# Kernel tuning notes

Measured on AMD Instinct MI355X. Metric: run time of the kernel, lower is better.

## Reference

```python
import jax, jax.numpy as jnp
import numpy as np

DIM = 128
NUM_HEADS = 2
WS = 8  # window_size


def setup_inputs() -> dict:
    key = jax.random.key(0)
    ks = jax.random.split(key, 8)
    B, C, H, W = 1, DIM, 64, 128  # W must equal DIM (proj acts on last spatial axis)
    w_scale = 1.0 / np.sqrt(DIM)
    return {
        "x": jax.random.normal(ks[0], (B, C, H, W), jnp.float32),
        "wavelet_features": jax.random.normal(ks[1], (B, C, H, W), jnp.float32),
        "Wq": jax.random.normal(ks[2], (DIM, DIM), jnp.float32) * w_scale,
        "bq": jnp.zeros((DIM,), jnp.float32),
        "Wk": jax.random.normal(ks[3], (DIM, DIM), jnp.float32) * w_scale,
        "bk": jnp.zeros((DIM,), jnp.float32),
        "Wv": jax.random.normal(ks[4], (DIM, DIM), jnp.float32) * w_scale,
        "bv": jnp.zeros((DIM,), jnp.float32),
        "Wp": jax.random.normal(ks[5], (DIM, DIM), jnp.float32) * w_scale,
        "bp": jnp.zeros((DIM,), jnp.float32),
    }


def _window_partition(t):
    # 'b c (h wh) (w ww) -> b (h w) (wh ww) c'
    B, C, H, W = t.shape
    h, w = H // WS, W // WS
    t = t.reshape(B, C, h, WS, w, WS)
    t = t.transpose(0, 2, 4, 3, 5, 1)  # B,h,w,wh,ww,C
    return t.reshape(B, h * w, WS * WS, C)


def reference(x, wavelet_features, Wq, bq, Wk, bk, Wv, bv, Wp, bp):
    B, C, H, W = x.shape
    hd = C // NUM_HEADS
    scale = hd ** (-0.5)

    xw = _window_partition(x)                   # [B, nW, ws*ws, C]
    ww = _window_partition(wavelet_features)    # [B, nW, ws*ws, C]

    q = xw @ Wq.T + bq
    k = ww @ Wk.T + bk
    v = ww @ Wv.T + bv

    # NOTE: original code flattens windows+tokens together, so attention is
    # GLOBAL over all N = H*W tokens (window partition is just a permutation).
    N = q.shape[1] * q.shape[2]
    q = q.reshape(B, N, NUM_HEADS, hd).transpose(0, 2, 1, 3)  # [B,h,N,d]
    k = k.reshape(B, N, NUM_HEADS, hd).transpose(0, 2, 1, 3)
    v = v.reshape(B, N, NUM_HEADS, hd).transpose(0, 2, 1, 3)

    attn = jax.nn.softmax(jnp.einsum('bhnd,bhmd->bhnm', q, k) * scale, axis=-1)
    out = jnp.einsum('bhnm,bhmd->bhnd', attn, v)  # [B,h,N,d]
    out = out.transpose(0, 2, 1, 3).reshape(B, N, C)

    # 'b (h w) (wh ww) c -> b c (h wh) (w ww)'
    h, w = H // WS, W // WS
    out = out.reshape(B, h, w, WS, WS, C).transpose(0, 5, 1, 3, 2, 4).reshape(B, C, H, W)

    # Faithful quirk: proj Linear acts on the LAST axis (spatial W == dim).
    out = out @ Wp.T + bp
    return out
```

## Files before the change

kernel.cpp:

```cpp
#include <hip/hip_runtime.h>
#include <stdint.h>

typedef float    f32x4  __attribute__((ext_vector_type(4)));
typedef __bf16   bf16x8 __attribute__((ext_vector_type(8)));
typedef short    s16x8  __attribute__((ext_vector_type(8)));
typedef int      i32x4  __attribute__((ext_vector_type(4)));
typedef unsigned short u16x4 __attribute__((ext_vector_type(4)));

#define DEVINL __device__ __forceinline__

DEVINL unsigned short f2bf(float f) {
  unsigned u = __builtin_bit_cast(unsigned, f);
  return (unsigned short)((u + 0x7fffu + ((u >> 16) & 1u)) >> 16);
}

DEVINL f32x4 mfma16(bf16x8 a, bf16x8 b, f32x4 c) {
  return __builtin_amdgcn_mfma_f32_16x16x32_bf16(a, b, c, 0, 0, 0);
}

DEVINL bf16x8 lds_frag(const unsigned char* p) {
  return __builtin_bit_cast(bf16x8, *(const s16x8*)p);
}

template <int CTRL>
DEVINL float dppf(float x) {
  int xi = __builtin_bit_cast(int, x);
  return __builtin_bit_cast(float, __builtin_amdgcn_update_dpp(xi, xi, CTRL, 0xF, 0xF, true));
}
DEVINL float redmax16(float v) {
  v = fmaxf(v, dppf<0xB1>(v));
  v = fmaxf(v, dppf<0x4E>(v));
  v = fmaxf(v, dppf<0x141>(v));
  v = fmaxf(v, dppf<0x140>(v));
  return v;
}
DEVINL float redsum16(float v) {
  v += dppf<0xB1>(v);
  v += dppf<0x4E>(v);
  v += dppf<0x141>(v);
  v += dppf<0x140>(v);
  return v;
}

__global__ __launch_bounds__(256) void prep_w_kernel(
    const float* __restrict__ wq, const float* __restrict__ wk,
    const float* __restrict__ wv, const float* __restrict__ wp,
    unsigned short* __restrict__ wbf) {
  int id = blockIdx.x * 256 + threadIdx.x;
  int m = id >> 12;
  const float* src = (m == 0) ? wq : (m == 1) ? wk : (m == 2) ? wv : wp;
  f32x4 v = ((const f32x4*)src)[id & 4095];
  u16x4 o;
  o[0] = f2bf(v[0]); o[1] = f2bf(v[1]); o[2] = f2bf(v[2]); o[3] = f2bf(v[3]);
  ((u16x4*)wbf)[id] = o;
}

__global__ __launch_bounds__(256) void qkv_kernel(
    const float* __restrict__ x, const float* __restrict__ wav,
    const unsigned short* __restrict__ wbf,
    const float* __restrict__ bq, const float* __restrict__ bk, const float* __restrict__ bv,
    unsigned short* __restrict__ Qb, unsigned short* __restrict__ Kb,
    unsigned short* __restrict__ Vt) {
  __shared__ __align__(16) unsigned char sm[32768];
  const int tid = threadIdx.x;
  const int g = blockIdx.x >> 7;
  const int s0 = (blockIdx.x & 127) * 64;
  const float* srcm = (g == 0) ? x : wav;

  {
    const int c = tid >> 1, half = tid & 1;
    const float* xs = srcm + c * 8192 + s0 + half * 32;
#pragma unroll
    for (int i = 0; i < 8; ++i) {
      f32x4 vx = *(const f32x4*)(xs + i * 4);
#pragma unroll
      for (int j = 0; j < 4; ++j) {
        int s = half * 32 + i * 4 + j;
        int off = (c * 2) ^ ((s & 7) << 4);
        *(unsigned short*)(sm + s * 256 + off) = f2bf(vx[j]);
      }
    }
  }
  __syncthreads();

  const int w = tid >> 6, l = tid & 63, lr = l & 15, lh = l >> 4;
  const int arow = w * 16 + lr;
  const int aswz = (lr & 7) << 4;

  const unsigned char* asrc = sm + arow * 256;
  const unsigned char* wsrc = (const unsigned char*)wbf + g * 32768;
  f32x4 acc[8];
#pragma unroll
  for (int jt = 0; jt < 8; ++jt) acc[jt] = (f32x4){0.f, 0.f, 0.f, 0.f};
#pragma unroll
  for (int ks = 0; ks < 4; ++ks) {
    bf16x8 a = lds_frag(asrc + ((ks * 64 + lh * 16) ^ aswz));
#pragma unroll
    for (int jt = 0; jt < 8; ++jt) {
      bf16x8 bb = __builtin_bit_cast(
          bf16x8, *(const s16x8*)(wsrc + (jt * 16 + lr) * 256 + ks * 64 + lh * 16));
      acc[jt] = mfma16(a, bb, acc[jt]);
    }
  }
  if (g < 2) {
    const float* bias = g ? bk : bq;
    unsigned short* outp = g ? Kb : Qb;
#pragma unroll
    for (int jt = 0; jt < 8; ++jt) {
      float bb = bias[jt * 16 + lr];
#pragma unroll
      for (int r = 0; r < 4; ++r) {
        int row = s0 + w * 16 + lh * 4 + r;
        outp[row * 128 + jt * 16 + lr] = f2bf(acc[jt][r] + bb);
      }
    }
  } else {
    unsigned char* sm2 = sm + 16384;
#pragma unroll
    for (int jt = 0; jt < 8; ++jt) {
      float bb = bv[jt * 16 + lr];
#pragma unroll
      for (int r = 0; r < 4; ++r) {
        int jj = jt * 16 + lr;
        int sl = w * 16 + lh * 4 + r;
        *(unsigned short*)(sm2 + jj * 128 + ((sl * 2) ^ ((jj & 7) << 4))) =
            f2bf(acc[jt][r] + bb);
      }
    }
    __syncthreads();
#pragma unroll
    for (int g2 = 0; g2 < 4; ++g2) {
      int jj = w * 32 + g2 * 8 + (l >> 3);
      s16x8 row = *(const s16x8*)(sm2 + jj * 128 + (((l & 7) * 16) ^ ((jj & 7) << 4)));
      *(s16x8*)(Vt + jj * 8192 + s0 + (l & 7) * 8) = row;
    }
  }
}

__global__ __launch_bounds__(256) void attn_kernel(
    const unsigned short* __restrict__ Qb, const unsigned short* __restrict__ Kb,
    const unsigned short* __restrict__ Vt, float* __restrict__ Opart,
    float* __restrict__ Ml, float* __restrict__ Ll, int TPS) {
  __shared__ __align__(16) unsigned char sm[24576];
  const int tid = threadIdx.x;
  const int bid = blockIdx.x;
  const int hq = bid & 255, sp = bid >> 8;
  const int h = hq & 1, q0 = (hq >> 1) * 64;
  const int t0 = sp * TPS;
  const int w = tid >> 6, l = tid & 63, lr = l & 15, lh = l >> 4;
  const int lswz = (lr & 7) << 4;

  bf16x8 qf[2];
#pragma unroll
  for (int ks = 0; ks < 2; ++ks)
    qf[ks] = __builtin_bit_cast(
        bf16x8, *(const s16x8*)(Qb + (q0 + w * 16 + lr) * 128 + h * 64 + ks * 32 + lh * 8));

  f32x4 acc[4];
  float m_[4], l_[4];
#pragma unroll
  for (int i = 0; i < 4; ++i) { acc[i] = (f32x4){0.f,0.f,0.f,0.f}; m_[i] = -1e30f; l_[i] = 0.f; }

  int srow[2], soff[2], sldsoff[2];
#pragma unroll
  for (int i = 0; i < 2; ++i) {
    int ch = tid + i * 256;
    srow[i] = ch >> 3;
    soff[i] = (ch & 7) * 8;
    sldsoff[i] = srow[i] * 128 + ((soff[i] * 2) ^ ((srow[i] & 7) << 4));
  }

  {
#pragma unroll
    for (int i = 0; i < 2; ++i) {
      i32x4 kv = *(const i32x4*)(Kb + (t0 * 64 + srow[i]) * 128 + h * 64 + soff[i]);
      i32x4 vv = *(const i32x4*)(Vt + (h * 64 + srow[i]) * 8192 + t0 * 64 + soff[i]);
      *(i32x4*)(sm + sldsoff[i]) = kv;
      *(i32x4*)(sm + 8192 + sldsoff[i]) = vv;
    }
  }
  __syncthreads();

  const float sc = 0.18033688011112042f;

  for (int tt = 0; tt < TPS; ++tt) {
    const int t = t0 + tt;
    i32x4 nk[2], nv[2];
    if (tt < TPS - 1) {
#pragma unroll
      for (int i = 0; i < 2; ++i) {
        nk[i] = *(const i32x4*)(Kb + ((t + 1) * 64 + srow[i]) * 128 + h * 64 + soff[i]);
        nv[i] = *(const i32x4*)(Vt + (h * 64 + srow[i]) * 8192 + (t + 1) * 64 + soff[i]);
      }
    }
    const unsigned char* kb = sm;
    const unsigned char* vb = sm + 8192;
    unsigned char* pb = sm + 16384;

    f32x4 s4[4];
#pragma unroll
    for (int nt = 0; nt < 4; ++nt) s4[nt] = (f32x4){0.f,0.f,0.f,0.f};
#pragma unroll
    for (int ks = 0; ks < 2; ++ks) {
#pragma unroll
      for (int nt = 0; nt < 4; ++nt) {
        bf16x8 kf = lds_frag(kb + (nt * 16 + lr) * 128 + ((ks * 64 + lh * 16) ^ lswz));
        s4[nt] = mfma16(qf[ks], kf, s4[nt]);
      }
    }

    float p[4][4];
#pragma unroll
    for (int r = 0; r < 4; ++r) {
      float mx = fmaxf(fmaxf(s4[0][r], s4[1][r]), fmaxf(s4[2][r], s4[3][r]));
      mx = redmax16(mx) * sc;
      float mn = fmaxf(m_[r], mx);
      float al = __builtin_amdgcn_exp2f(m_[r] - mn);
      m_[r] = mn;
      float rs = 0.f;
#pragma unroll
      for (int nt = 0; nt < 4; ++nt) {
        p[nt][r] = __builtin_amdgcn_exp2f(fmaf(s4[nt][r], sc, -mn));
        rs += p[nt][r];
      }
      rs = redsum16(rs);
      l_[r] = l_[r] * al + rs;
#pragma unroll
      for (int ct = 0; ct < 4; ++ct) acc[ct][r] *= al;
    }

    const int qrow = w * 16 + lh * 4;
#pragma unroll
    for (int r = 0; r < 4; r += 2) {
      int qa = qrow + r, qb2 = qrow + r + 1;
      unsigned char* rowa = pb + qa * 128;
      unsigned char* rowb = pb + qb2 * 128;
      int swza = (qa & 7) << 4, swzb = (qb2 & 7) << 4;
#pragma unroll
      for (int nt = 0; nt < 4; ++nt) {
        unsigned u;
        asm("v_cvt_pk_bf16_f32 %0, %1, %2" : "=v"(u) : "v"(p[nt][r]), "v"(p[nt][r + 1]));
        int koff = (nt * 16 + lr) * 2;
        *(unsigned short*)(rowa + (koff ^ swza)) = (unsigned short)u;
        *(unsigned short*)(rowb + (koff ^ swzb)) = (unsigned short)(u >> 16);
      }
    }
    asm volatile("s_waitcnt lgkmcnt(0)" ::: "memory");
    __builtin_amdgcn_sched_barrier(0);

    bf16x8 pa[2];
#pragma unroll
    for (int ks = 0; ks < 2; ++ks)
      pa[ks] = lds_frag(pb + (w * 16 + lr) * 128 + ((ks * 64 + lh * 16) ^ lswz));
#pragma unroll
    for (int ks = 0; ks < 2; ++ks) {
#pragma unroll
      for (int ct = 0; ct < 4; ++ct) {
        bf16x8 vf = lds_frag(vb + (ct * 16 + lr) * 128 + ((ks * 64 + lh * 16) ^ lswz));
        acc[ct] = mfma16(pa[ks], vf, acc[ct]);
      }
    }

    __syncthreads();
    if (tt < TPS - 1) {
#pragma unroll
      for (int i = 0; i < 2; ++i) {
        *(i32x4*)(sm + sldsoff[i]) = nk[i];
        *(i32x4*)(sm + 8192 + sldsoff[i]) = nv[i];
      }
    }
    __syncthreads();
  }

  float* op = Opart + (size_t)bid * 4096;
#pragma unroll
  for (int ct = 0; ct < 4; ++ct) {
#pragma unroll
    for (int r = 0; r < 4; ++r) {
      int q = w * 16 + lh * 4 + r;
      op[q * 64 + ct * 16 + lr] = acc[ct][r];
    }
  }
  if (lr == 0) {
#pragma unroll
    for (int r = 0; r < 4; ++r) {
      int q = w * 16 + lh * 4 + r;
      Ml[bid * 64 + q] = m_[r];
      Ll[bid * 64 + q] = l_[r];
    }
  }
}

__global__ __launch_bounds__(256) void combine_kernel(
    const float* __restrict__ Opart, const float* __restrict__ Ml,
    const float* __restrict__ Ll, unsigned short* __restrict__ Ot, int S) {
  __shared__ float wgt_s[8][32];
  __shared__ float rinv_s[32];
  __shared__ unsigned short lt[64][34];
  const int bid = blockIdx.x;
  const int hq = bid >> 1, half = bid & 1;
  const int h = hq & 1, q0 = (hq >> 1) * 64;
  const int t = threadIdx.x;

  if (t < 32) {
    int qg = half * 32 + t;
    float m8[8];
    float M = -1e30f;
    for (int sp = 0; sp < S; ++sp) {
      m8[sp] = Ml[(size_t)(sp * 256 + hq) * 64 + qg];
      M = fmaxf(M, m8[sp]);
    }
    float L = 0.f;
    for (int sp = 0; sp < S; ++sp) {
      float wv = __builtin_amdgcn_exp2f(m8[sp] - M);
      wgt_s[sp][t] = wv;
      L += Ll[(size_t)(sp * 256 + hq) * 64 + qg] * wv;
    }
    rinv_s[t] = 1.0f / L;
  }
  __syncthreads();

  const int q = t >> 3;
  const int dc = t & 7;
  const int qg = half * 32 + q;
  f32x4 o0 = (f32x4){0.f,0.f,0.f,0.f}, o1 = (f32x4){0.f,0.f,0.f,0.f};
  for (int sp = 0; sp < S; ++sp) {
    const f32x4* src =
        (const f32x4*)(Opart + (size_t)(sp * 256 + hq) * 4096 + qg * 64 + dc * 8);
    float wv = wgt_s[sp][q];
    o0 += src[0] * wv;
    o1 += src[1] * wv;
  }
  float rinv = rinv_s[q];
#pragma unroll
  for (int j = 0; j < 4; ++j) lt[dc * 8 + j][q] = f2bf(o0[j] * rinv);
#pragma unroll
  for (int j = 0; j < 4; ++j) lt[dc * 8 + 4 + j][q] = f2bf(o1[j] * rinv);
  __syncthreads();

  const int d = t >> 2, q8 = (t & 3) * 8;
  unsigned short tmp[8];
#pragma unroll
  for (int j = 0; j < 8; ++j) tmp[j] = lt[d][q8 + j];
  *(s16x8*)(Ot + (size_t)(h * 64 + d) * 8192 + q0 + half * 32 + q8) = *(s16x8*)tmp;
}

__global__ __launch_bounds__(256) void proj_kernel(
    const unsigned short* __restrict__ Ot, const unsigned short* __restrict__ wbf,
    const float* __restrict__ bp, float* __restrict__ out) {
  __shared__ __align__(16) unsigned char sm[16384];
  const int tid = threadIdx.x;
  const int r0 = blockIdx.x * 64;
#pragma unroll
  for (int i = 0; i < 4; ++i) {
    int chk = tid + 256 * i;
    i32x4 v = *(const i32x4*)(Ot + r0 * 128 + chk * 8);
    int row = chk >> 4, off = (chk & 15) * 16;
    *(i32x4*)(sm + row * 256 + (off ^ ((row & 7) << 4))) = v;
  }
  __syncthreads();
  const int w = tid >> 6, l = tid & 63, lr = l & 15, lh = l >> 4;
  f32x4 acc[8];
#pragma unroll
  for (int jt = 0; jt < 8; ++jt) acc[jt] = (f32x4){0.f, 0.f, 0.f, 0.f};
  const unsigned char* wsrc = (const unsigned char*)wbf + 3 * 32768;
#pragma unroll
  for (int ks = 0; ks < 4; ++ks) {
    bf16x8 a = lds_frag(sm + (w * 16 + lr) * 256 + ((ks * 64 + lh * 16) ^ ((lr & 7) << 4)));
#pragma unroll
    for (int jt = 0; jt < 8; ++jt) {
      bf16x8 bb = __builtin_bit_cast(
          bf16x8, *(const s16x8*)(wsrc + (jt * 16 + lr) * 256 + ks * 64 + lh * 16));
      acc[jt] = mfma16(a, bb, acc[jt]);
    }
  }
#pragma unroll
  for (int jt = 0; jt < 8; ++jt) {
    float bb = bp[jt * 16 + lr];
#pragma unroll
    for (int r = 0; r < 4; ++r)
      out[(r0 + w * 16 + lh * 4 + r) * 128 + jt * 16 + lr] = acc[jt][r] + bb;
  }
}

extern "C" void kernel_launch(void* const* d_in, const int* in_sizes, int n_in,
                              void* d_out, int out_size, void* d_ws, size_t ws_size,
                              hipStream_t stream) {
  const float* x   = (const float*)d_in[0];
  const float* wav = (const float*)d_in[1];
  const float* Wq  = (const float*)d_in[2];
  const float* bq  = (const float*)d_in[3];
  const float* Wk  = (const float*)d_in[4];
  const float* bk  = (const float*)d_in[5];
  const float* Wv  = (const float*)d_in[6];
  const float* bv  = (const float*)d_in[7];
  const float* Wp  = (const float*)d_in[8];
  const float* bp  = (const float*)d_in[9];
  (void)in_sizes; (void)n_in; (void)out_size;

  unsigned char* ws = (unsigned char*)d_ws;
  unsigned short* Qb  = (unsigned short*)(ws);
  unsigned short* Kb  = (unsigned short*)(ws + 2097152);
  unsigned short* Vt  = (unsigned short*)(ws + 4194304);
  unsigned short* Ot  = (unsigned short*)(ws + 6291456);
  unsigned short* Wbf = (unsigned short*)(ws + 8388608);

  const size_t pbase = 8519680;
  int S = 8;
  while (S > 1 && pbase + (size_t)S * 4325376 > ws_size) S >>= 1;
  float* Opart = (float*)(ws + pbase);
  float* Ml    = (float*)(ws + pbase + (size_t)S * 4194304);
  float* Ll    = (float*)(ws + pbase + (size_t)S * 4194304 + (size_t)S * 65536);
  const int TPS = 128 / S;

  prep_w_kernel<<<64, 256, 0, stream>>>(Wq, Wk, Wv, Wp, Wbf);
  qkv_kernel<<<384, 256, 0, stream>>>(x, wav, Wbf, bq, bk, bv, Qb, Kb, Vt);
  attn_kernel<<<256 * S, 256, 0, stream>>>(Qb, Kb, Vt, Opart, Ml, Ll, TPS);
  combine_kernel<<<512, 256, 0, stream>>>(Opart, Ml, Ll, Ot, S);
  proj_kernel<<<128, 256, 0, stream>>>(Ot, Wbf, bp, (float*)d_out);
}
```

Before: 122.9 us.

## Double attention KV tile to 128 keys and compute row sums via MFMA

The attention kernel now processes 128 keys per iteration instead of 64, halving loop iterations and the number of online-softmax rescale steps and barriers per block. The P tile overwrites the K region in LDS after an added barrier, so shared memory grows to 32 KB instead of 48 KB. The softmax row sum is no longer a DPP shuffle reduction; it is computed by an extra MFMA of P against a ones vector, using the bf16-rounded P values. This adds register pressure (8 score tiles) and an extra sync per iteration.

```diff
diff --git a/kernel.cpp b/kernel.cpp
--- a/kernel.cpp
+++ b/kernel.cpp
@@ -32,13 +32,6 @@
   v = fmaxf(v, dppf<0x4E>(v));
   v = fmaxf(v, dppf<0x141>(v));
   v = fmaxf(v, dppf<0x140>(v));
-  return v;
-}
-DEVINL float redsum16(float v) {
-  v += dppf<0xB1>(v);
-  v += dppf<0x4E>(v);
-  v += dppf<0x141>(v);
-  v += dppf<0x140>(v);
   return v;
 }
 
@@ -140,13 +133,13 @@
 __global__ __launch_bounds__(256) void attn_kernel(
     const unsigned short* __restrict__ Qb, const unsigned short* __restrict__ Kb,
     const unsigned short* __restrict__ Vt, float* __restrict__ Opart,
-    float* __restrict__ Ml, float* __restrict__ Ll, int TPS) {
-  __shared__ __align__(16) unsigned char sm[24576];
+    float* __restrict__ Ml, float* __restrict__ Ll, int NIT) {
+  __shared__ __align__(16) unsigned char sm[32768];
   const int tid = threadIdx.x;
   const int bid = blockIdx.x;
   const int hq = bid & 255, sp = bid >> 8;
   const int h = hq & 1, q0 = (hq >> 1) * 64;
-  const int t0 = sp * TPS;
+  const int t0 = sp * NIT;
   const int w = tid >> 6, l = tid & 63, lr = l & 15, lh = l >> 4;
   const int lswz = (lr & 7) << 4;
 
@@ -156,91 +149,94 @@
     qf[ks] = __builtin_bit_cast(
         bf16x8, *(const s16x8*)(Qb + (q0 + w * 16 + lr) * 128 + h * 64 + ks * 32 + lh * 8));
 
+  const s16x8 ones_i = {0x3F80, 0x3F80, 0x3F80, 0x3F80, 0x3F80, 0x3F80, 0x3F80, 0x3F80};
+  const bf16x8 onesf = __builtin_bit_cast(bf16x8, ones_i);
+
   f32x4 acc[4];
   float m_[4], l_[4];
 #pragma unroll
   for (int i = 0; i < 4; ++i) { acc[i] = (f32x4){0.f,0.f,0.f,0.f}; m_[i] = -1e30f; l_[i] = 0.f; }
 
-  int srow[2], soff[2], sldsoff[2];
-#pragma unroll
-  for (int i = 0; i < 2; ++i) {
+  int srow[4], soff[4], kldsoff[4], vrow[4], voff[4], vldsoff[4];
+#pragma unroll
+  for (int i = 0; i < 4; ++i) {
     int ch = tid + i * 256;
     srow[i] = ch >> 3;
     soff[i] = (ch & 7) * 8;
-    sldsoff[i] = srow[i] * 128 + ((soff[i] * 2) ^ ((srow[i] & 7) << 4));
+    kldsoff[i] = srow[i] * 128 + ((soff[i] * 2) ^ ((srow[i] & 7) << 4));
+    vrow[i] = ch >> 4;
+    voff[i] = (ch & 15) * 8;
+    vldsoff[i] = 16384 + vrow[i] * 256 + ((voff[i] * 2) ^ ((vrow[i] & 7) << 4));
   }
 
   {
 #pragma unroll
-    for (int i = 0; i < 2; ++i) {
-      i32x4 kv = *(const i32x4*)(Kb + (t0 * 64 + srow[i]) * 128 + h * 64 + soff[i]);
-      i32x4 vv = *(const i32x4*)(Vt + (h * 64 + srow[i]) * 8192 + t0 * 64 + soff[i]);
-      *(i32x4*)(sm + sldsoff[i]) = kv;
-      *(i32x4*)(sm + 8192 + sldsoff[i]) = vv;
+    for (int i = 0; i < 4; ++i) {
+      i32x4 kv = *(const i32x4*)(Kb + (size_t)(t0 * 128 + srow[i]) * 128 + h * 64 + soff[i]);
+      i32x4 vv = *(const i32x4*)(Vt + (size_t)(h * 64 + vrow[i]) * 8192 + t0 * 128 + voff[i]);
+      *(i32x4*)(sm + kldsoff[i]) = kv;
+      *(i32x4*)(sm + vldsoff[i]) = vv;
     }
   }
   __syncthreads();
 
   const float sc = 0.18033688011112042f;
 
-  for (int tt = 0; tt < TPS; ++tt) {
-    const int t = t0 + tt;
-    i32x4 nk[2], nv[2];
-    if (tt < TPS - 1) {
-#pragma unroll
-      for (int i = 0; i < 2; ++i) {
-        nk[i] = *(const i32x4*)(Kb + ((t + 1) * 64 + srow[i]) * 128 + h * 64 + soff[i]);
-        nv[i] = *(const i32x4*)(Vt + (h * 64 + srow[i]) * 8192 + (t + 1) * 64 + soff[i]);
-      }
-    }
-    const unsigned char* kb = sm;
-    const unsigned char* vb = sm + 8192;
-    unsigned char* pb = sm + 16384;
-
-    f32x4 s4[4];
-#pragma unroll
-    for (int nt = 0; nt < 4; ++nt) s4[nt] = (f32x4){0.f,0.f,0.f,0.f};
+  for (int tt = 0; tt < NIT; ++tt) {
+    i32x4 nk[4], nv[4];
+    if (tt < NIT - 1) {
+#pragma unroll
+      for (int i = 0; i < 4; ++i) {
+        nk[i] = *(const i32x4*)(Kb + (size_t)((t0 + tt + 1) * 128 + srow[i]) * 128 + h * 64 + soff[i]);
+        nv[i] = *(const i32x4*)(Vt + (size_t)(h * 64 + vrow[i]) * 8192 + (t0 + tt + 1) * 128 + voff[i]);
+      }
+    }
+    const unsigned char* kp = sm;
+    const unsigned char* vb = sm + 16384;
+
+    f32x4 s8[8];
+#pragma unroll
+    for (int nt = 0; nt < 8; ++nt) s8[nt] = (f32x4){0.f,0.f,0.f,0.f};
 #pragma unroll
     for (int ks = 0; ks < 2; ++ks) {
 #pragma unroll
-      for (int nt = 0; nt < 4; ++nt) {
-        bf16x8 kf = lds_frag(kb + (nt * 16 + lr) * 128 + ((ks * 64 + lh * 16) ^ lswz));
-        s4[nt] = mfma16(qf[ks], kf, s4[nt]);
-      }
-    }
-
-    float p[4][4];
+      for (int nt = 0; nt < 8; ++nt) {
+        bf16x8 kf = lds_frag(kp + (nt * 16 + lr) * 128 + ((ks * 64 + lh * 16) ^ lswz));
+        s8[nt] = mfma16(qf[ks], kf, s8[nt]);
+      }
+    }
+
 #pragma unroll
     for (int r = 0; r < 4; ++r) {
-      float mx = fmaxf(fmaxf(s4[0][r], s4[1][r]), fmaxf(s4[2][r], s4[3][r]));
+      float mx = s8[0][r];
+#pragma unroll
+      for (int nt = 1; nt < 8; ++nt) mx = fmaxf(mx, s8[nt][r]);
       mx = redmax16(mx) * sc;
       float mn = fmaxf(m_[r], mx);
       float al = __builtin_amdgcn_exp2f(m_[r] - mn);
       m_[r] = mn;
-      float rs = 0.f;
-#pragma unroll
-      for (int nt = 0; nt < 4; ++nt) {
-        p[nt][r] = __builtin_amdgcn_exp2f(fmaf(s4[nt][r], sc, -mn));
-        rs += p[nt][r];
-      }
-      rs = redsum16(rs);
-      l_[r] = l_[r] * al + rs;
+      l_[r] *= al;
+#pragma unroll
+      for (int nt = 0; nt < 8; ++nt)
+        s8[nt][r] = __builtin_amdgcn_exp2f(fmaf(s8[nt][r], sc, -mn));
 #pragma unroll
       for (int ct = 0; ct < 4; ++ct) acc[ct][r] *= al;
     }
+
+    __syncthreads();
 
     const int qrow = w * 16 + lh * 4;
 #pragma unroll
     for (int r = 0; r < 4; r += 2) {
       int qa = qrow + r, qb2 = qrow + r + 1;
-      unsigned char* rowa = pb + qa * 128;
-      unsigned char* rowb = pb + qb2 * 128;
+      unsigned char* rowa = sm + qa * 256;
+      unsigned char* rowb = sm + qb2 * 256;
       int swza = (qa & 7) << 4, swzb = (qb2 & 7) << 4;
 #pragma unroll
-      for (int nt = 0; nt < 4; ++nt) {
+      for (int nt = 0; nt < 8; ++nt) {
         unsigned u;
-        asm("v_cvt_pk_bf16_f32 %0, %1, %2" : "=v"(u) : "v"(p[nt][r]), "v"(p[nt][r + 1]));
-        int koff = (nt * 16 + lr) * 2;
+        asm("v_cvt_pk_bf16_f32 %0, %1, %2" : "=v"(u) : "v"(s8[nt][r]), "v"(s8[nt][r + 1]));
+        int koff = nt * 32 + lr * 2;
         *(unsigned short*)(rowa + (koff ^ swza)) = (unsigned short)u;
         *(unsigned short*)(rowb + (koff ^ swzb)) = (unsigned short)(u >> 16);
       }
@@ -248,25 +244,29 @@
     asm volatile("s_waitcnt lgkmcnt(0)" ::: "memory");
     __builtin_amdgcn_sched_barrier(0);
 
-    bf16x8 pa[2];
-#pragma unroll
-    for (int ks = 0; ks < 2; ++ks)
-      pa[ks] = lds_frag(pb + (w * 16 + lr) * 128 + ((ks * 64 + lh * 16) ^ lswz));
-#pragma unroll
-    for (int ks = 0; ks < 2; ++ks) {
+    bf16x8 pa[4];
+#pragma unroll
+    for (int ks = 0; ks < 4; ++ks)
+      pa[ks] = lds_frag(kp + (w * 16 + lr) * 256 + ((ks * 64 + lh * 16) ^ lswz));
+    f32x4 lt4 = (f32x4){0.f,0.f,0.f,0.f};
+#pragma unroll
+    for (int ks = 0; ks < 4; ++ks) {
+      lt4 = mfma16(pa[ks], onesf, lt4);
 #pragma unroll
       for (int ct = 0; ct < 4; ++ct) {
-        bf16x8 vf = lds_frag(vb + (ct * 16 + lr) * 128 + ((ks * 64 + lh * 16) ^ lswz));
+        bf16x8 vf = lds_frag(vb + (ct * 16 + lr) * 256 + ((ks * 64 + lh * 16) ^ lswz));
         acc[ct] = mfma16(pa[ks], vf, acc[ct]);
       }
     }
+#pragma unroll
+    for (int r = 0; r < 4; ++r) l_[r] += lt4[r];
 
     __syncthreads();
-    if (tt < TPS - 1) {
-#pragma unroll
-      for (int i = 0; i < 2; ++i) {
-        *(i32x4*)(sm + sldsoff[i]) = nk[i];
-        *(i32x4*)(sm + 8192 + sldsoff[i]) = nv[i];
+    if (tt < NIT - 1) {
+#pragma unroll
+      for (int i = 0; i < 4; ++i) {
+        *(i32x4*)(sm + kldsoff[i]) = nk[i];
+        *(i32x4*)(sm + vldsoff[i]) = nv[i];
       }
     }
     __syncthreads();
@@ -411,11 +411,11 @@
   float* Opart = (float*)(ws + pbase);
   float* Ml    = (float*)(ws + pbase + (size_t)S * 4194304);
   float* Ll    = (float*)(ws + pbase + (size_t)S * 4194304 + (size_t)S * 65536);
-  const int TPS = 128 / S;
+  const int NIT = 64 / S;
 
   prep_w_kernel<<<64, 256, 0, stream>>>(Wq, Wk, Wv, Wp, Wbf);
   qkv_kernel<<<384, 256, 0, stream>>>(x, wav, Wbf, bq, bk, bv, Qb, Kb, Vt);
-  attn_kernel<<<256 * S, 256, 0, stream>>>(Qb, Kb, Vt, Opart, Ml, Ll, TPS);
+  attn_kernel<<<256 * S, 256, 0, stream>>>(Qb, Kb, Vt, Opart, Ml, Ll, NIT);
   combine_kernel<<<512, 256, 0, stream>>>(Opart, Ml, Ll, Ot, S);
   proj_kernel<<<128, 256, 0, stream>>>(Ot, Wbf, bp, (float*)d_out);
 }
```

Result: no change. 124.2 us (+1.1%).

## Process two query tiles per attention block and compute row sums via MFMA

Applied to the files above, without the earlier changes.

Each attention block now handles 128 queries (two 64-row tiles) against the same staged K/V tiles, so each K/V load into shared memory is reused twice and the grid is halved. The softmax row-sum reduction through DPP shuffles is replaced by an MFMA of the bf16 probabilities against a ones vector. In exchange, register pressure and LDS use go up, which may lower occupancy. The row sums now come from bf16-rounded probabilities, a slight numeric change.

```diff
diff --git a/kernel.cpp b/kernel.cpp
--- a/kernel.cpp
+++ b/kernel.cpp
@@ -32,13 +32,6 @@
   v = fmaxf(v, dppf<0x4E>(v));
   v = fmaxf(v, dppf<0x141>(v));
   v = fmaxf(v, dppf<0x140>(v));
-  return v;
-}
-DEVINL float redsum16(float v) {
-  v += dppf<0xB1>(v);
-  v += dppf<0x4E>(v);
-  v += dppf<0x141>(v);
-  v += dppf<0x140>(v);
   return v;
 }
 
@@ -140,26 +133,36 @@
 __global__ __launch_bounds__(256) void attn_kernel(
     const unsigned short* __restrict__ Qb, const unsigned short* __restrict__ Kb,
     const unsigned short* __restrict__ Vt, float* __restrict__ Opart,
-    float* __restrict__ Ml, float* __restrict__ Ll, int TPS) {
-  __shared__ __align__(16) unsigned char sm[24576];
+    float* __restrict__ Ml, float* __restrict__ Ll, int NIT) {
+  __shared__ __align__(16) unsigned char sm[32768];
   const int tid = threadIdx.x;
   const int bid = blockIdx.x;
-  const int hq = bid & 255, sp = bid >> 8;
-  const int h = hq & 1, q0 = (hq >> 1) * 64;
-  const int t0 = sp * TPS;
+  const int sp = bid >> 7, g = bid & 127;
+  const int h = g & 1, qb2 = g >> 1;
+  const int q0 = qb2 * 128;
+  const int t0 = sp * NIT;
   const int w = tid >> 6, l = tid & 63, lr = l & 15, lh = l >> 4;
   const int lswz = (lr & 7) << 4;
 
-  bf16x8 qf[2];
-#pragma unroll
-  for (int ks = 0; ks < 2; ++ks)
-    qf[ks] = __builtin_bit_cast(
+  bf16x8 qfA[2], qfB[2];
+#pragma unroll
+  for (int ks = 0; ks < 2; ++ks) {
+    qfA[ks] = __builtin_bit_cast(
         bf16x8, *(const s16x8*)(Qb + (q0 + w * 16 + lr) * 128 + h * 64 + ks * 32 + lh * 8));
-
-  f32x4 acc[4];
-  float m_[4], l_[4];
-#pragma unroll
-  for (int i = 0; i < 4; ++i) { acc[i] = (f32x4){0.f,0.f,0.f,0.f}; m_[i] = -1e30f; l_[i] = 0.f; }
+    qfB[ks] = __builtin_bit_cast(
+        bf16x8, *(const s16x8*)(Qb + (q0 + 64 + w * 16 + lr) * 128 + h * 64 + ks * 32 + lh * 8));
+  }
+
+  const s16x8 ones_i = {0x3F80, 0x3F80, 0x3F80, 0x3F80, 0x3F80, 0x3F80, 0x3F80, 0x3F80};
+  const bf16x8 onesf = __builtin_bit_cast(bf16x8, ones_i);
+
+  f32x4 accA[4], accB[4];
+  float mA[4], lA[4], mB[4], lB[4];
+#pragma unroll
+  for (int i = 0; i < 4; ++i) {
+    accA[i] = (f32x4){0.f,0.f,0.f,0.f}; accB[i] = (f32x4){0.f,0.f,0.f,0.f};
+    mA[i] = -1e30f; lA[i] = 0.f; mB[i] = -1e30f; lB[i] = 0.f;
+  }
 
   int srow[2], soff[2], sldsoff[2];
 #pragma unroll
@@ -183,10 +186,10 @@
 
   const float sc = 0.18033688011112042f;
 
-  for (int tt = 0; tt < TPS; ++tt) {
+  for (int tt = 0; tt < NIT; ++tt) {
     const int t = t0 + tt;
     i32x4 nk[2], nv[2];
-    if (tt < TPS - 1) {
+    if (tt < NIT - 1) {
 #pragma unroll
       for (int i = 0; i < 2; ++i) {
         nk[i] = *(const i32x4*)(Kb + ((t + 1) * 64 + srow[i]) * 128 + h * 64 + soff[i]);
@@ -195,74 +198,94 @@
     }
     const unsigned char* kb = sm;
     const unsigned char* vb = sm + 8192;
-    unsigned char* pb = sm + 16384;
-
-    f32x4 s4[4];
-#pragma unroll
-    for (int nt = 0; nt < 4; ++nt) s4[nt] = (f32x4){0.f,0.f,0.f,0.f};
+    unsigned char* pbA = sm + 16384;
+    unsigned char* pbB = sm + 24576;
+
+    f32x4 sA[4], sB[4];
+#pragma unroll
+    for (int nt = 0; nt < 4; ++nt) { sA[nt] = (f32x4){0.f,0.f,0.f,0.f}; sB[nt] = (f32x4){0.f,0.f,0.f,0.f}; }
 #pragma unroll
     for (int ks = 0; ks < 2; ++ks) {
 #pragma unroll
       for (int nt = 0; nt < 4; ++nt) {
         bf16x8 kf = lds_frag(kb + (nt * 16 + lr) * 128 + ((ks * 64 + lh * 16) ^ lswz));
-        s4[nt] = mfma16(qf[ks], kf, s4[nt]);
-      }
-    }
-
-    float p[4][4];
+        sA[nt] = mfma16(qfA[ks], kf, sA[nt]);
+        sB[nt] = mfma16(qfB[ks], kf, sB[nt]);
+      }
+    }
+
 #pragma unroll
     for (int r = 0; r < 4; ++r) {
-      float mx = fmaxf(fmaxf(s4[0][r], s4[1][r]), fmaxf(s4[2][r], s4[3][r]));
+      float mx = fmaxf(fmaxf(sA[0][r], sA[1][r]), fmaxf(sA[2][r], sA[3][r]));
       mx = redmax16(mx) * sc;
-      float mn = fmaxf(m_[r], mx);
-      float al = __builtin_amdgcn_exp2f(m_[r] - mn);
-      m_[r] = mn;
-      float rs = 0.f;
+      float mn = fmaxf(mA[r], mx);
+      float al = __builtin_amdgcn_exp2f(mA[r] - mn);
+      mA[r] = mn;
+      lA[r] *= al;
+#pragma unroll
+      for (int nt = 0; nt < 4; ++nt)
+        sA[nt][r] = __builtin_amdgcn_exp2f(fmaf(sA[nt][r], sc, -mn));
+#pragma unroll
+      for (int ct = 0; ct < 4; ++ct) accA[ct][r] *= al;
+    }
+#pragma unroll
+    for (int r = 0; r < 4; ++r) {
+      float mx = fmaxf(fmaxf(sB[0][r], sB[1][r]), fmaxf(sB[2][r], sB[3][r]));
+      mx = redmax16(mx) * sc;
+      float mn = fmaxf(mB[r], mx);
+      float al = __builtin_amdgcn_exp2f(mB[r] - mn);
+      mB[r] = mn;
+      lB[r] *= al;
+#pragma unroll
+      for (int nt = 0; nt < 4; ++nt)
+        sB[nt][r] = __builtin_amdgcn_exp2f(fmaf(sB[nt][r], sc, -mn));
+#pragma unroll
+      for (int ct = 0; ct < 4; ++ct) accB[ct][r] *= al;
+    }
+
+    const int qrow = w * 16 + lh * 4;
+#pragma unroll
+    for (int r = 0; r < 4; r += 2) {
+      int qa = qrow + r, qb = qrow + r + 1;
+      int swza = (qa & 7) << 4, swzb = (qb & 7) << 4;
 #pragma unroll
       for (int nt = 0; nt < 4; ++nt) {
-        p[nt][r] = __builtin_amdgcn_exp2f(fmaf(s4[nt][r], sc, -mn));
-        rs += p[nt][r];
-      }
-      rs = redsum16(rs);
-      l_[r] = l_[r] * al + rs;
-#pragma unroll
-      for (int ct = 0; ct < 4; ++ct) acc[ct][r] *= al;
-    }
-
-    const int qrow = w * 16 + lh * 4;
-#pragma unroll
-    for (int r = 0; r < 4; r += 2) {
-      int qa = qrow + r, qb2 = qrow + r + 1;
-      unsigned char* rowa = pb + qa * 128;
-      unsigned char* rowb = pb + qb2 * 128;
-      int swza = (qa & 7) << 4, swzb = (qb2 & 7) << 4;
-#pragma unroll
-      for (int nt = 0; nt < 4; ++nt) {
+        int koff = (nt * 16 + lr) * 2;
         unsigned u;
-        asm("v_cvt_pk_bf16_f32 %0, %1, %2" : "=v"(u) : "v"(p[nt][r]), "v"(p[nt][r + 1]));
-        int koff = (nt * 16 + lr) * 2;
-        *(unsigned short*)(rowa + (koff ^ swza)) = (unsigned short)u;
-        *(unsigned short*)(rowb + (koff ^ swzb)) = (unsigned short)(u >> 16);
+        asm("v_cvt_pk_bf16_f32 %0, %1, %2" : "=v"(u) : "v"(sA[nt][r]), "v"(sA[nt][r + 1]));
+        *(unsigned short*)(pbA + qa * 128 + (koff ^ swza)) = (unsigned short)u;
+        *(unsigned short*)(pbA + qb * 128 + (koff ^ swzb)) = (unsigned short)(u >> 16);
+        asm("v_cvt_pk_bf16_f32 %0, %1, %2" : "=v"(u) : "v"(sB[nt][r]), "v"(sB[nt][r + 1]));
+        *(unsigned short*)(pbB + qa * 128 + (koff ^ swza)) = (unsigned short)u;
+        *(unsigned short*)(pbB + qb * 128 + (koff ^ swzb)) = (unsigned short)(u >> 16);
       }
     }
     asm volatile("s_waitcnt lgkmcnt(0)" ::: "memory");
     __builtin_amdgcn_sched_barrier(0);
 
-    bf16x8 pa[2];
-#pragma unroll
-    for (int ks = 0; ks < 2; ++ks)
-      pa[ks] = lds_frag(pb + (w * 16 + lr) * 128 + ((ks * 64 + lh * 16) ^ lswz));
+    bf16x8 paA[2], paB[2];
 #pragma unroll
     for (int ks = 0; ks < 2; ++ks) {
+      paA[ks] = lds_frag(pbA + (w * 16 + lr) * 128 + ((ks * 64 + lh * 16) ^ lswz));
+      paB[ks] = lds_frag(pbB + (w * 16 + lr) * 128 + ((ks * 64 + lh * 16) ^ lswz));
+    }
+    f32x4 ltA = (f32x4){0.f,0.f,0.f,0.f}, ltB = (f32x4){0.f,0.f,0.f,0.f};
+#pragma unroll
+    for (int ks = 0; ks < 2; ++ks) {
+      ltA = mfma16(paA[ks], onesf, ltA);
+      ltB = mfma16(paB[ks], onesf, ltB);
 #pragma unroll
       for (int ct = 0; ct < 4; ++ct) {
         bf16x8 vf = lds_frag(vb + (ct * 16 + lr) * 128 + ((ks * 64 + lh * 16) ^ lswz));
-        acc[ct] = mfma16(pa[ks], vf, acc[ct]);
-      }
-    }
+        accA[ct] = mfma16(paA[ks], vf, accA[ct]);
+        accB[ct] = mfma16(paB[ks], vf, accB[ct]);
+      }
+    }
+#pragma unroll
+    for (int r = 0; r < 4; ++r) { lA[r] += ltA[r]; lB[r] += ltB[r]; }
 
     __syncthreads();
-    if (tt < TPS - 1) {
+    if (tt < NIT - 1) {
 #pragma unroll
       for (int i = 0; i < 2; ++i) {
         *(i32x4*)(sm + sldsoff[i]) = nk[i];
@@ -272,21 +295,27 @@
     __syncthreads();
   }
 
-  float* op = Opart + (size_t)bid * 4096;
+  const size_t pbA_i = (size_t)sp * 256 + 4 * qb2 + h;
+  const size_t pbB_i = (size_t)sp * 256 + 4 * qb2 + 2 + h;
+  float* opA = Opart + pbA_i * 4096;
+  float* opB = Opart + pbB_i * 4096;
 #pragma unroll
   for (int ct = 0; ct < 4; ++ct) {
 #pragma unroll
     for (int r = 0; r < 4; ++r) {
       int q = w * 16 + lh * 4 + r;
-      op[q * 64 + ct * 16 + lr] = acc[ct][r];
+      opA[q * 64 + ct * 16 + lr] = accA[ct][r];
+      opB[q * 64 + ct * 16 + lr] = accB[ct][r];
     }
   }
   if (lr == 0) {
 #pragma unroll
     for (int r = 0; r < 4; ++r) {
       int q = w * 16 + lh * 4 + r;
-      Ml[bid * 64 + q] = m_[r];
-      Ll[bid * 64 + q] = l_[r];
+      Ml[pbA_i * 64 + q] = mA[r];
+      Ll[pbA_i * 64 + q] = lA[r];
+      Ml[pbB_i * 64 + q] = mB[r];
+      Ll[pbB_i * 64 + q] = lB[r];
     }
   }
 }
@@ -411,11 +440,11 @@
   float* Opart = (float*)(ws + pbase);
   float* Ml    = (float*)(ws + pbase + (size_t)S * 4194304);
   float* Ll    = (float*)(ws + pbase + (size_t)S * 4194304 + (size_t)S * 65536);
-  const int TPS = 128 / S;
+  const int NIT = 128 / S;
 
   prep_w_kernel<<<64, 256, 0, stream>>>(Wq, Wk, Wv, Wp, Wbf);
   qkv_kernel<<<384, 256, 0, stream>>>(x, wav, Wbf, bq, bk, bv, Qb, Kb, Vt);
-  attn_kernel<<<256 * S, 256, 0, stream>>>(Qb, Kb, Vt, Opart, Ml, Ll, TPS);
+  attn_kernel<<<128 * S, 256, 0, stream>>>(Qb, Kb, Vt, Opart, Ml, Ll, NIT);
   combine_kernel<<<512, 256, 0, stream>>>(Opart, Ml, Ll, Ot, S);
   proj_kernel<<<128, 256, 0, stream>>>(Ot, Wbf, bp, (float*)d_out);
 }
```

New measurement: 123.1 us. No clear change (+0.2%).
